# Kernel optimization log

Hardware: AMD Instinct MI355X
Metric: run time of the kernel (lower is better)

## Reference

```python
import jax, jax.numpy as jnp
import numpy as np

EMBED_DIM = 1024
NUM_HEADS = 16
HEAD_DIM = EMBED_DIM // NUM_HEADS


def setup_inputs() -> dict:
    key = jax.random.key(0)
    ks = jax.random.split(key, 11)
    B, S, E = 2, 2048, EMBED_DIM
    s = 1.0 / np.sqrt(E)
    inp = {
        "query": jax.random.normal(ks[0], (B, S, E), dtype=jnp.float32),
        "key": jax.random.normal(ks[1], (B, S, E), dtype=jnp.float32),
        "value": jax.random.normal(ks[2], (B, S, E), dtype=jnp.float32),
        # nn.Linear weights stored as [out, in]; y = x @ W.T + b
        "q_w": jax.random.normal(ks[3], (E, E), dtype=jnp.float32) * s,
        "q_b": jax.random.normal(ks[4], (E,), dtype=jnp.float32) * s,
        "k_w": jax.random.normal(ks[5], (E, E), dtype=jnp.float32) * s,
        "k_b": jax.random.normal(ks[6], (E,), dtype=jnp.float32) * s,
        "v_w": jax.random.normal(ks[7], (E, E), dtype=jnp.float32) * s,
        "v_b": jax.random.normal(ks[8], (E,), dtype=jnp.float32) * s,
        "o_w": jax.random.normal(ks[9], (E, E), dtype=jnp.float32) * s,
        "o_b": jax.random.normal(ks[10], (E,), dtype=jnp.float32) * s,
    }
    return inp


def _split_heads(x):
    B, S, E = x.shape
    return x.reshape(B, S, NUM_HEADS, HEAD_DIM).transpose(0, 2, 1, 3)  # [B,H,S,Dh]


def reference(query, key, value, q_w, q_b, k_w, k_b, v_w, v_b, o_w, o_b):
    Q = _split_heads(query @ q_w.T + q_b)
    K = _split_heads(key @ k_w.T + k_b)
    V = _split_heads(value @ v_w.T + v_b)
    scale = 1.0 / jnp.sqrt(jnp.float32(HEAD_DIM))
    scores = jnp.einsum("bhqd,bhkd->bhqk", Q, K) * scale  # [B,H,S,S]
    attn_weights = jax.nn.softmax(scores, axis=-1)
    # dropout in eval mode -> identity
    attn_out = jnp.einsum("bhqk,bhkd->bhqd", attn_weights, V)
    B, H, S, Dh = attn_out.shape
    attn_out = attn_out.transpose(0, 2, 1, 3).reshape(B, S, H * Dh)
    output = attn_out @ o_w.T + o_b
    return (output, attn_weights)
```

## Files before the change

kernel.cpp:

```cpp
#include <hip/hip_runtime.h>
#include <cstdint>
#include <cstddef>

#define S_LEN 2048
#define EMB   1024
#define NH    16
#define DH    64

typedef unsigned short u16;
typedef __attribute__((ext_vector_type(8))) short bf16x8;
typedef __attribute__((ext_vector_type(4))) float f32x4;

__device__ __forceinline__ u16 f2bf(float f) {
  unsigned int u = __float_as_uint(f);
  u = (u + 0x7fffu + ((u >> 16) & 1u)) >> 16;
  return (u16)u;
}

__device__ __forceinline__ void gload16(const void* g, void* l) {
  __builtin_amdgcn_global_load_lds(
      (const __attribute__((address_space(1))) unsigned int*)g,
      (__attribute__((address_space(3))) unsigned int*)l, 16, 0, 0);
}

__global__ void cvt_bf16(const float* __restrict__ src, u16* __restrict__ dst, int n4) {
  int i = blockIdx.x * blockDim.x + threadIdx.x;
  if (i >= n4) return;
  float4 v = ((const float4*)src)[i];
  ushort4 o;
  o.x = f2bf(v.x); o.y = f2bf(v.y); o.z = f2bf(v.z); o.w = f2bf(v.w);
  ((ushort4*)dst)[i] = o;
}

__global__ __launch_bounds__(256) void gemm_bt(
    const u16* __restrict__ A, const u16* __restrict__ B,
    const float* __restrict__ bias, u16* __restrict__ out,
    float* __restrict__ outf, int K, float scale, int mode) {
  __shared__ u16 a_sm[128 * 64];
  __shared__ u16 b_sm[128 * 64];
  const int tid = threadIdx.x;
  const int lane = tid & 63, wv = tid >> 6;
  const int l16 = lane & 15, quad = lane >> 4;
  const int m0 = blockIdx.y * 128, n0 = blockIdx.x * 128;
  const int wrow = (wv >> 1) * 64, wcol = (wv & 1) * 64;
  const f32x4 fzero = {0.f, 0.f, 0.f, 0.f};

  f32x4 acc[4][4];
#pragma unroll
  for (int i = 0; i < 4; i++)
#pragma unroll
    for (int j = 0; j < 4; j++) acc[i][j] = fzero;

  const int srow = lane >> 3;
  const int scol = (lane & 7) * 8;

  for (int k0 = 0; k0 < K; k0 += 64) {
#pragma unroll
    for (int i = 0; i < 4; i++) {
      int rr = (wv * 4 + i) * 8 + srow;
      int ldso = ((wv * 4 + i) * 64 + lane) * 8;
      gload16(&A[(size_t)(m0 + rr) * K + k0 + scol], &a_sm[ldso]);
      gload16(&B[(size_t)(n0 + rr) * K + k0 + scol], &b_sm[ldso]);
    }
    __syncthreads();
#pragma unroll
    for (int ks = 0; ks < 2; ks++) {
      bf16x8 af[4], bff[4];
#pragma unroll
      for (int t = 0; t < 4; t++) {
        af[t]  = *(const bf16x8*)&a_sm[(wrow + t * 16 + l16) * 64 + ks * 32 + quad * 8];
        bff[t] = *(const bf16x8*)&b_sm[(wcol + t * 16 + l16) * 64 + ks * 32 + quad * 8];
      }
#pragma unroll
      for (int mt = 0; mt < 4; mt++)
#pragma unroll
        for (int nt = 0; nt < 4; nt++)
          acc[mt][nt] = __builtin_amdgcn_mfma_f32_16x16x32_bf16(af[mt], bff[nt], acc[mt][nt], 0, 0, 0);
    }
    __syncthreads();
  }

#pragma unroll
  for (int nt = 0; nt < 4; nt++) {
    const int n = n0 + wcol + nt * 16 + l16;
    const float bv = bias[n];
#pragma unroll
    for (int mt = 0; mt < 4; mt++) {
      const int mb = m0 + wrow + mt * 16 + quad * 4;
      if (mode == 0) {
#pragma unroll
        for (int r = 0; r < 4; r++) {
          int m = mb + r;
          int b = m >> 11, s = m & (S_LEN - 1);
          int h = n >> 6, d = n & 63;
          out[((size_t)(b * NH + h) * S_LEN + s) * DH + d] = f2bf((acc[mt][nt][r] + bv) * scale);
        }
      } else if (mode == 1) {
        int b = mb >> 11, s = mb & (S_LEN - 1);
        int h = n >> 6, d = n & 63;
        ushort4 o;
        o.x = f2bf((acc[mt][nt][0] + bv) * scale);
        o.y = f2bf((acc[mt][nt][1] + bv) * scale);
        o.z = f2bf((acc[mt][nt][2] + bv) * scale);
        o.w = f2bf((acc[mt][nt][3] + bv) * scale);
        *(ushort4*)&out[((size_t)(b * NH + h) * DH + d) * S_LEN + s] = o;
      } else {
#pragma unroll
        for (int r = 0; r < 4; r++) {
          int m = mb + r;
          outf[(size_t)m * EMB + n] = acc[mt][nt][r] + bv;
        }
      }
    }
  }
}

__global__ __launch_bounds__(256) void attn_pass_a(
    const u16* __restrict__ Qb, const u16* __restrict__ Kb, float* __restrict__ invl) {
  __shared__ u16 q_sm[128 * 64];
  __shared__ u16 k_sm[128 * 64];
  const int tid = threadIdx.x;
  const int lane = tid & 63, wv = tid >> 6;
  const int l16 = lane & 15, quad = lane >> 4;
  const int bh = blockIdx.y, q0 = blockIdx.x * 128;
  const u16* Qp = Qb + (size_t)bh * S_LEN * DH;
  const u16* Kp = Kb + (size_t)bh * S_LEN * DH;

#pragma unroll
  for (int i = 0; i < 4; i++) {
    int off = ((wv * 4 + i) * 64 + lane) * 8;
    gload16(Qp + (size_t)q0 * DH + off, &q_sm[off]);
  }
  __syncthreads();

  bf16x8 aq[2][2];
#pragma unroll
  for (int mt = 0; mt < 2; mt++)
#pragma unroll
    for (int ks = 0; ks < 2; ks++)
      aq[mt][ks] = *(const bf16x8*)&q_sm[(wv * 32 + mt * 16 + l16) * 64 + ks * 32 + quad * 8];

  float racc[8];
#pragma unroll
  for (int i = 0; i < 8; i++) racc[i] = 0.f;
  const f32x4 fzero = {0.f, 0.f, 0.f, 0.f};

  for (int kt0 = 0; kt0 < S_LEN; kt0 += 128) {
#pragma unroll
    for (int i = 0; i < 4; i++) {
      int off = ((wv * 4 + i) * 64 + lane) * 8;
      gload16(Kp + (size_t)kt0 * DH + off, &k_sm[off]);
    }
    __syncthreads();
#pragma unroll
    for (int nt = 0; nt < 8; nt++) {
      bf16x8 bk0 = *(const bf16x8*)&k_sm[(nt * 16 + l16) * 64 + quad * 8];
      bf16x8 bk1 = *(const bf16x8*)&k_sm[(nt * 16 + l16) * 64 + 32 + quad * 8];
#pragma unroll
      for (int mt = 0; mt < 2; mt++) {
        f32x4 c = fzero;
        c = __builtin_amdgcn_mfma_f32_16x16x32_bf16(aq[mt][0], bk0, c, 0, 0, 0);
        c = __builtin_amdgcn_mfma_f32_16x16x32_bf16(aq[mt][1], bk1, c, 0, 0, 0);
#pragma unroll
        for (int r = 0; r < 4; r++) racc[mt * 4 + r] += __expf(c[r]);
      }
    }
    __syncthreads();
  }
#pragma unroll
  for (int i = 0; i < 8; i++) {
    racc[i] += __shfl_xor(racc[i], 1);
    racc[i] += __shfl_xor(racc[i], 2);
    racc[i] += __shfl_xor(racc[i], 4);
    racc[i] += __shfl_xor(racc[i], 8);
  }
  if (l16 == 0) {
#pragma unroll
    for (int mt = 0; mt < 2; mt++)
#pragma unroll
      for (int r = 0; r < 4; r++)
        invl[(size_t)bh * S_LEN + q0 + wv * 32 + mt * 16 + quad * 4 + r] = 1.0f / racc[mt * 4 + r];
  }
}

__global__ __launch_bounds__(256) void attn_pass_b(
    const u16* __restrict__ Qb, const u16* __restrict__ Kb,
    const u16* __restrict__ Vt, const float* __restrict__ invl,
    float* __restrict__ wout, u16* __restrict__ aout) {
  __shared__ u16 k_sm[128 * 64];
  __shared__ u16 vt_sm[64 * 128];
  __shared__ u16 p_sm[128 * 128];
  __shared__ float il_sm[128];
  const int tid = threadIdx.x;
  const int lane = tid & 63, wv = tid >> 6;
  const int l16 = lane & 15, quad = lane >> 4;
  const int bh = blockIdx.y, q0 = blockIdx.x * 128;
  const u16* Qp = Qb + (size_t)bh * S_LEN * DH;
  const u16* Kp = Kb + (size_t)bh * S_LEN * DH;
  const u16* Vp = Vt + (size_t)bh * DH * S_LEN;
  const f32x4 fzero = {0.f, 0.f, 0.f, 0.f};

#pragma unroll
  for (int i = 0; i < 4; i++) {
    int off = ((wv * 4 + i) * 64 + lane) * 8;
    gload16(Qp + (size_t)q0 * DH + off, &k_sm[off]);
  }
  if (tid < 128) il_sm[tid] = invl[(size_t)bh * S_LEN + q0 + tid];
  __syncthreads();
  bf16x8 aq[2][2];
#pragma unroll
  for (int mt = 0; mt < 2; mt++)
#pragma unroll
    for (int ks = 0; ks < 2; ks++)
      aq[mt][ks] = *(const bf16x8*)&k_sm[(wv * 32 + mt * 16 + l16) * 64 + ks * 32 + quad * 8];
  float il[2][4];
#pragma unroll
  for (int mt = 0; mt < 2; mt++)
#pragma unroll
    for (int r = 0; r < 4; r++)
      il[mt][r] = il_sm[wv * 32 + mt * 16 + quad * 4 + r];
  __syncthreads();

  f32x4 oacc[8];
#pragma unroll
  for (int i = 0; i < 8; i++) oacc[i] = fzero;

  const size_t rowbase = ((size_t)bh * S_LEN + q0) * S_LEN;

  for (int kt0 = 0; kt0 < S_LEN; kt0 += 128) {
#pragma unroll
    for (int i = 0; i < 4; i++) {
      int off = ((wv * 4 + i) * 64 + lane) * 8;
      gload16(Kp + (size_t)kt0 * DH + off, &k_sm[off]);
      gload16(Vp + (size_t)((wv * 4 + i) * 4 + quad) * S_LEN + kt0 + l16 * 8, &vt_sm[off]);
    }
    __syncthreads();

#pragma unroll
    for (int nt = 0; nt < 8; nt++) {
      bf16x8 bk0 = *(const bf16x8*)&k_sm[(nt * 16 + l16) * 64 + quad * 8];
      bf16x8 bk1 = *(const bf16x8*)&k_sm[(nt * 16 + l16) * 64 + 32 + quad * 8];
#pragma unroll
      for (int mt = 0; mt < 2; mt++) {
        f32x4 c = fzero;
        c = __builtin_amdgcn_mfma_f32_16x16x32_bf16(aq[mt][0], bk0, c, 0, 0, 0);
        c = __builtin_amdgcn_mfma_f32_16x16x32_bf16(aq[mt][1], bk1, c, 0, 0, 0);
#pragma unroll
        for (int r = 0; r < 4; r++) {
          float w = __expf(c[r]) * il[mt][r];
          int qlocal = wv * 32 + mt * 16 + quad * 4 + r;
          wout[rowbase + (size_t)qlocal * S_LEN + kt0 + nt * 16 + l16] = w;
          p_sm[qlocal * 128 + nt * 16 + l16] = f2bf(w);
        }
      }
    }
    __syncthreads();

    bf16x8 av[4];
#pragma unroll
    for (int ks = 0; ks < 4; ks++)
      av[ks] = *(const bf16x8*)&vt_sm[(wv * 16 + l16) * 128 + ks * 32 + quad * 8];
#pragma unroll
    for (int nt = 0; nt < 8; nt++)
#pragma unroll
      for (int ks = 0; ks < 4; ks++) {
        bf16x8 bp = *(const bf16x8*)&p_sm[(nt * 16 + l16) * 128 + ks * 32 + quad * 8];
        oacc[nt] = __builtin_amdgcn_mfma_f32_16x16x32_bf16(av[ks], bp, oacc[nt], 0, 0, 0);
      }
    __syncthreads();
  }

  const int b = bh >> 4, h = bh & 15;
#pragma unroll
  for (int nt = 0; nt < 8; nt++) {
    int s = q0 + nt * 16 + l16;
    int d0 = wv * 16 + quad * 4;
    ushort4 o;
    o.x = f2bf(oacc[nt][0]);
    o.y = f2bf(oacc[nt][1]);
    o.z = f2bf(oacc[nt][2]);
    o.w = f2bf(oacc[nt][3]);
    *(ushort4*)&aout[(size_t)(b * S_LEN + s) * EMB + h * DH + d0] = o;
  }
}

extern "C" void kernel_launch(void* const* d_in, const int* in_sizes, int n_in,
                              void* d_out, int out_size, void* d_ws, size_t ws_size,
                              hipStream_t stream) {
  const float* q_f  = (const float*)d_in[0];
  const float* k_f  = (const float*)d_in[1];
  const float* v_f  = (const float*)d_in[2];
  const float* qw_f = (const float*)d_in[3];
  const float* qb_f = (const float*)d_in[4];
  const float* kw_f = (const float*)d_in[5];
  const float* kb_f = (const float*)d_in[6];
  const float* vw_f = (const float*)d_in[7];
  const float* vb_f = (const float*)d_in[8];
  const float* ow_f = (const float*)d_in[9];
  const float* ob_f = (const float*)d_in[10];

  uint8_t* wsb = (uint8_t*)d_ws;
  u16*   qb   = (u16*)(wsb + (size_t)(0u  << 20));
  u16*   kb   = (u16*)(wsb + (size_t)(8u  << 20));
  u16*   vt   = (u16*)(wsb + (size_t)(16u << 20));
  u16*   xq   = (u16*)(wsb + (size_t)(24u << 20));
  u16*   xk   = (u16*)(wsb + (size_t)(32u << 20));
  u16*   xv   = (u16*)(wsb + (size_t)(40u << 20));
  u16*   wq   = (u16*)(wsb + (size_t)(48u << 20));
  u16*   wk   = (u16*)(wsb + (size_t)(50u << 20));
  u16*   wvw  = (u16*)(wsb + (size_t)(52u << 20));
  u16*   wo   = (u16*)(wsb + (size_t)(54u << 20));
  float* invl = (float*)(wsb + (size_t)(56u << 20));
  u16*   ao   = (u16*)(wsb + (size_t)(57u << 20));

  const int NA4 = (2 * S_LEN * EMB) / 4;
  const int NW4 = (EMB * EMB) / 4;
  cvt_bf16<<<NA4 / 256, 256, 0, stream>>>(q_f, xq, NA4);
  cvt_bf16<<<NA4 / 256, 256, 0, stream>>>(k_f, xk, NA4);
  cvt_bf16<<<NA4 / 256, 256, 0, stream>>>(v_f, xv, NA4);
  cvt_bf16<<<NW4 / 256, 256, 0, stream>>>(qw_f, wq, NW4);
  cvt_bf16<<<NW4 / 256, 256, 0, stream>>>(kw_f, wk, NW4);
  cvt_bf16<<<NW4 / 256, 256, 0, stream>>>(vw_f, wvw, NW4);
  cvt_bf16<<<NW4 / 256, 256, 0, stream>>>(ow_f, wo, NW4);

  dim3 gp(8, 32);
  gemm_bt<<<gp, 256, 0, stream>>>(xq, wq, qb_f, qb, nullptr, EMB, 0.125f, 0);
  gemm_bt<<<gp, 256, 0, stream>>>(xk, wk, kb_f, kb, nullptr, EMB, 1.0f, 0);
  gemm_bt<<<gp, 256, 0, stream>>>(xv, wvw, vb_f, vt, nullptr, EMB, 1.0f, 1);

  dim3 ga(16, 32);
  attn_pass_a<<<ga, 256, 0, stream>>>(qb, kb, invl);

  float* outp = (float*)d_out;
  attn_pass_b<<<ga, 256, 0, stream>>>(qb, kb, vt, invl, outp + (size_t)2 * S_LEN * EMB, ao);

  gemm_bt<<<gp, 256, 0, stream>>>(ao, wo, ob_f, nullptr, outp, EMB, 1.0f, 2);
}
```

Before: 856.2 us.

## Merge conversions, batch QKV GEMMs, fuse softmax-denominator pass into attention kernel

Replaces seven conversion launches with one combined kernel and the three projection GEMMs with a single launch using a z-grid dimension. Folds the row-sum pass into the attention kernel, so each block computes its own softmax denominators before the output pass. This removes launch overhead and the invl round trip and raises GEMM grid occupancy. Each attention block still makes two sweeps over K, and register pressure rises in the fused kernel.

```diff
diff --git a/kernel.cpp b/kernel.cpp
--- a/kernel.cpp
+++ b/kernel.cpp
@@ -23,21 +23,39 @@
       (__attribute__((address_space(3))) unsigned int*)l, 16, 0, 0);
 }
 
-__global__ void cvt_bf16(const float* __restrict__ src, u16* __restrict__ dst, int n4) {
+__global__ void cvt_all(
+    const float* __restrict__ q_f, const float* __restrict__ k_f, const float* __restrict__ v_f,
+    const float* __restrict__ qw_f, const float* __restrict__ kw_f,
+    const float* __restrict__ vw_f, const float* __restrict__ ow_f,
+    u16* __restrict__ xq, u16* __restrict__ xk, u16* __restrict__ xv,
+    u16* __restrict__ wq, u16* __restrict__ wk, u16* __restrict__ wv, u16* __restrict__ wo) {
   int i = blockIdx.x * blockDim.x + threadIdx.x;
-  if (i >= n4) return;
-  float4 v = ((const float4*)src)[i];
+  const float* src;
+  u16* dst;
+  int off;
+  if (i < (3 << 20)) {
+    int r = i >> 20;
+    off = i & ((1 << 20) - 1);
+    src = (r == 0) ? q_f : (r == 1) ? k_f : v_f;
+    dst = (r == 0) ? xq  : (r == 1) ? xk  : xv;
+  } else {
+    int j = i - (3 << 20);
+    int r = j >> 18;
+    off = j & ((1 << 18) - 1);
+    src = (r == 0) ? qw_f : (r == 1) ? kw_f : (r == 2) ? vw_f : ow_f;
+    dst = (r == 0) ? wq   : (r == 1) ? wk   : (r == 2) ? wv   : wo;
+  }
+  float4 v = ((const float4*)src)[off];
   ushort4 o;
   o.x = f2bf(v.x); o.y = f2bf(v.y); o.z = f2bf(v.z); o.w = f2bf(v.w);
-  ((ushort4*)dst)[i] = o;
-}
-
-__global__ __launch_bounds__(256) void gemm_bt(
+  ((ushort4*)dst)[off] = o;
+}
+
+__device__ __forceinline__ void gemm_tile(
+    u16* a_sm, u16* b_sm,
     const u16* __restrict__ A, const u16* __restrict__ B,
     const float* __restrict__ bias, u16* __restrict__ out,
     float* __restrict__ outf, int K, float scale, int mode) {
-  __shared__ u16 a_sm[128 * 64];
-  __shared__ u16 b_sm[128 * 64];
   const int tid = threadIdx.x;
   const int lane = tid & 63, wv = tid >> 6;
   const int l16 = lane & 15, quad = lane >> 4;
@@ -115,82 +133,38 @@
   }
 }
 
-__global__ __launch_bounds__(256) void attn_pass_a(
-    const u16* __restrict__ Qb, const u16* __restrict__ Kb, float* __restrict__ invl) {
-  __shared__ u16 q_sm[128 * 64];
-  __shared__ u16 k_sm[128 * 64];
-  const int tid = threadIdx.x;
-  const int lane = tid & 63, wv = tid >> 6;
-  const int l16 = lane & 15, quad = lane >> 4;
-  const int bh = blockIdx.y, q0 = blockIdx.x * 128;
-  const u16* Qp = Qb + (size_t)bh * S_LEN * DH;
-  const u16* Kp = Kb + (size_t)bh * S_LEN * DH;
-
-#pragma unroll
-  for (int i = 0; i < 4; i++) {
-    int off = ((wv * 4 + i) * 64 + lane) * 8;
-    gload16(Qp + (size_t)q0 * DH + off, &q_sm[off]);
-  }
-  __syncthreads();
-
-  bf16x8 aq[2][2];
-#pragma unroll
-  for (int mt = 0; mt < 2; mt++)
-#pragma unroll
-    for (int ks = 0; ks < 2; ks++)
-      aq[mt][ks] = *(const bf16x8*)&q_sm[(wv * 32 + mt * 16 + l16) * 64 + ks * 32 + quad * 8];
-
-  float racc[8];
-#pragma unroll
-  for (int i = 0; i < 8; i++) racc[i] = 0.f;
-  const f32x4 fzero = {0.f, 0.f, 0.f, 0.f};
-
-  for (int kt0 = 0; kt0 < S_LEN; kt0 += 128) {
-#pragma unroll
-    for (int i = 0; i < 4; i++) {
-      int off = ((wv * 4 + i) * 64 + lane) * 8;
-      gload16(Kp + (size_t)kt0 * DH + off, &k_sm[off]);
-    }
-    __syncthreads();
-#pragma unroll
-    for (int nt = 0; nt < 8; nt++) {
-      bf16x8 bk0 = *(const bf16x8*)&k_sm[(nt * 16 + l16) * 64 + quad * 8];
-      bf16x8 bk1 = *(const bf16x8*)&k_sm[(nt * 16 + l16) * 64 + 32 + quad * 8];
-#pragma unroll
-      for (int mt = 0; mt < 2; mt++) {
-        f32x4 c = fzero;
-        c = __builtin_amdgcn_mfma_f32_16x16x32_bf16(aq[mt][0], bk0, c, 0, 0, 0);
-        c = __builtin_amdgcn_mfma_f32_16x16x32_bf16(aq[mt][1], bk1, c, 0, 0, 0);
-#pragma unroll
-        for (int r = 0; r < 4; r++) racc[mt * 4 + r] += __expf(c[r]);
-      }
-    }
-    __syncthreads();
-  }
-#pragma unroll
-  for (int i = 0; i < 8; i++) {
-    racc[i] += __shfl_xor(racc[i], 1);
-    racc[i] += __shfl_xor(racc[i], 2);
-    racc[i] += __shfl_xor(racc[i], 4);
-    racc[i] += __shfl_xor(racc[i], 8);
-  }
-  if (l16 == 0) {
-#pragma unroll
-    for (int mt = 0; mt < 2; mt++)
-#pragma unroll
-      for (int r = 0; r < 4; r++)
-        invl[(size_t)bh * S_LEN + q0 + wv * 32 + mt * 16 + quad * 4 + r] = 1.0f / racc[mt * 4 + r];
-  }
-}
-
-__global__ __launch_bounds__(256) void attn_pass_b(
+__global__ __launch_bounds__(256) void gemm_qkv(
+    const u16* __restrict__ xq, const u16* __restrict__ xk, const u16* __restrict__ xv,
+    const u16* __restrict__ wq, const u16* __restrict__ wk, const u16* __restrict__ wv,
+    const float* __restrict__ qb_f, const float* __restrict__ kb_f, const float* __restrict__ vb_f,
+    u16* __restrict__ qo, u16* __restrict__ ko, u16* __restrict__ vt) {
+  __shared__ u16 a_sm[128 * 64];
+  __shared__ u16 b_sm[128 * 64];
+  const int z = blockIdx.z;
+  const u16* A = (z == 0) ? xq : (z == 1) ? xk : xv;
+  const u16* B = (z == 0) ? wq : (z == 1) ? wk : wv;
+  const float* bias = (z == 0) ? qb_f : (z == 1) ? kb_f : vb_f;
+  u16* out = (z == 0) ? qo : (z == 1) ? ko : vt;
+  float scale = (z == 0) ? 0.125f : 1.0f;
+  int mode = (z == 2) ? 1 : 0;
+  gemm_tile(a_sm, b_sm, A, B, bias, out, nullptr, EMB, scale, mode);
+}
+
+__global__ __launch_bounds__(256) void gemm_o(
+    const u16* __restrict__ A, const u16* __restrict__ B,
+    const float* __restrict__ bias, float* __restrict__ outf) {
+  __shared__ u16 a_sm[128 * 64];
+  __shared__ u16 b_sm[128 * 64];
+  gemm_tile(a_sm, b_sm, A, B, bias, nullptr, outf, EMB, 1.0f, 2);
+}
+
+__global__ __launch_bounds__(256) void attn_fused(
     const u16* __restrict__ Qb, const u16* __restrict__ Kb,
-    const u16* __restrict__ Vt, const float* __restrict__ invl,
-    float* __restrict__ wout, u16* __restrict__ aout) {
+    const u16* __restrict__ Vt, float* __restrict__ wout,
+    u16* __restrict__ aout) {
   __shared__ u16 k_sm[128 * 64];
   __shared__ u16 vt_sm[64 * 128];
   __shared__ u16 p_sm[128 * 128];
-  __shared__ float il_sm[128];
   const int tid = threadIdx.x;
   const int lane = tid & 63, wv = tid >> 6;
   const int l16 = lane & 15, quad = lane >> 4;
@@ -205,7 +179,6 @@
     int off = ((wv * 4 + i) * 64 + lane) * 8;
     gload16(Qp + (size_t)q0 * DH + off, &k_sm[off]);
   }
-  if (tid < 128) il_sm[tid] = invl[(size_t)bh * S_LEN + q0 + tid];
   __syncthreads();
   bf16x8 aq[2][2];
 #pragma unroll
@@ -213,13 +186,46 @@
 #pragma unroll
     for (int ks = 0; ks < 2; ks++)
       aq[mt][ks] = *(const bf16x8*)&k_sm[(wv * 32 + mt * 16 + l16) * 64 + ks * 32 + quad * 8];
+  __syncthreads();
+
+  float racc[8];
+#pragma unroll
+  for (int i = 0; i < 8; i++) racc[i] = 0.f;
+
+  for (int kt0 = 0; kt0 < S_LEN; kt0 += 128) {
+#pragma unroll
+    for (int i = 0; i < 4; i++) {
+      int off = ((wv * 4 + i) * 64 + lane) * 8;
+      gload16(Kp + (size_t)kt0 * DH + off, &k_sm[off]);
+    }
+    __syncthreads();
+#pragma unroll
+    for (int nt = 0; nt < 8; nt++) {
+      bf16x8 bk0 = *(const bf16x8*)&k_sm[(nt * 16 + l16) * 64 + quad * 8];
+      bf16x8 bk1 = *(const bf16x8*)&k_sm[(nt * 16 + l16) * 64 + 32 + quad * 8];
+#pragma unroll
+      for (int mt = 0; mt < 2; mt++) {
+        f32x4 c = fzero;
+        c = __builtin_amdgcn_mfma_f32_16x16x32_bf16(aq[mt][0], bk0, c, 0, 0, 0);
+        c = __builtin_amdgcn_mfma_f32_16x16x32_bf16(aq[mt][1], bk1, c, 0, 0, 0);
+#pragma unroll
+        for (int r = 0; r < 4; r++) racc[mt * 4 + r] += __expf(c[r]);
+      }
+    }
+    __syncthreads();
+  }
+#pragma unroll
+  for (int i = 0; i < 8; i++) {
+    racc[i] += __shfl_xor(racc[i], 1);
+    racc[i] += __shfl_xor(racc[i], 2);
+    racc[i] += __shfl_xor(racc[i], 4);
+    racc[i] += __shfl_xor(racc[i], 8);
+  }
   float il[2][4];
 #pragma unroll
   for (int mt = 0; mt < 2; mt++)
 #pragma unroll
-    for (int r = 0; r < 4; r++)
-      il[mt][r] = il_sm[wv * 32 + mt * 16 + quad * 4 + r];
-  __syncthreads();
+    for (int r = 0; r < 4; r++) il[mt][r] = 1.0f / racc[mt * 4 + r];
 
   f32x4 oacc[8];
 #pragma unroll
@@ -310,29 +316,19 @@
   u16*   wk   = (u16*)(wsb + (size_t)(50u << 20));
   u16*   wvw  = (u16*)(wsb + (size_t)(52u << 20));
   u16*   wo   = (u16*)(wsb + (size_t)(54u << 20));
-  float* invl = (float*)(wsb + (size_t)(56u << 20));
   u16*   ao   = (u16*)(wsb + (size_t)(57u << 20));
 
-  const int NA4 = (2 * S_LEN * EMB) / 4;
-  const int NW4 = (EMB * EMB) / 4;
-  cvt_bf16<<<NA4 / 256, 256, 0, stream>>>(q_f, xq, NA4);
-  cvt_bf16<<<NA4 / 256, 256, 0, stream>>>(k_f, xk, NA4);
-  cvt_bf16<<<NA4 / 256, 256, 0, stream>>>(v_f, xv, NA4);
-  cvt_bf16<<<NW4 / 256, 256, 0, stream>>>(qw_f, wq, NW4);
-  cvt_bf16<<<NW4 / 256, 256, 0, stream>>>(kw_f, wk, NW4);
-  cvt_bf16<<<NW4 / 256, 256, 0, stream>>>(vw_f, wvw, NW4);
-  cvt_bf16<<<NW4 / 256, 256, 0, stream>>>(ow_f, wo, NW4);
+  cvt_all<<<(1 << 22) / 256, 256, 0, stream>>>(
+      q_f, k_f, v_f, qw_f, kw_f, vw_f, ow_f,
+      xq, xk, xv, wq, wk, wvw, wo);
+
+  dim3 gqkv(8, 32, 3);
+  gemm_qkv<<<gqkv, 256, 0, stream>>>(xq, xk, xv, wq, wk, wvw, qb_f, kb_f, vb_f, qb, kb, vt);
+
+  float* outp = (float*)d_out;
+  dim3 ga(16, 32);
+  attn_fused<<<ga, 256, 0, stream>>>(qb, kb, vt, outp + (size_t)2 * S_LEN * EMB, ao);
 
   dim3 gp(8, 32);
-  gemm_bt<<<gp, 256, 0, stream>>>(xq, wq, qb_f, qb, nullptr, EMB, 0.125f, 0);
-  gemm_bt<<<gp, 256, 0, stream>>>(xk, wk, kb_f, kb, nullptr, EMB, 1.0f, 0);
-  gemm_bt<<<gp, 256, 0, stream>>>(xv, wvw, vb_f, vt, nullptr, EMB, 1.0f, 1);
-
-  dim3 ga(16, 32);
-  attn_pass_a<<<ga, 256, 0, stream>>>(qb, kb, invl);
-
-  float* outp = (float*)d_out;
-  attn_pass_b<<<ga, 256, 0, stream>>>(qb, kb, vt, invl, outp + (size_t)2 * S_LEN * EMB, ao);
-
-  gemm_bt<<<gp, 256, 0, stream>>>(ao, wo, ob_f, nullptr, outp, EMB, 1.0f, 2);
-}
+  gemm_o<<<gp, 256, 0, stream>>>(ao, wo, ob_f, outp);
+}
```

Measured after the change: 802.7 us. 6.2% less time.
